# Kernel tuning notes

Measured on AMD Instinct MI355X. Metric: run time of the kernel, lower is better.

## Reference

```python
import jax, jax.numpy as jnp
import numpy as np

N_USERS = 50000
N_ITEMS = 150000
N = N_USERS + N_ITEMS
N_EDGES = 1250000
D = 64
N_LAYERS = 3


def setup_inputs() -> dict:
    key = jax.random.key(0)
    ks = jax.random.split(key, 7)
    edge_src = jax.random.randint(ks[0], (N_EDGES,), 0, N, dtype=jnp.int32)
    edge_dst = jax.random.randint(ks[1], (N_EDGES,), 0, N, dtype=jnp.int32)
    edge_weight = jax.random.uniform(ks[2], (N_EDGES,), dtype=jnp.float32)
    user_emb = jax.random.normal(ks[3], (N_USERS, D), dtype=jnp.float32) * 0.1
    item_emb = jax.random.normal(ks[4], (N_ITEMS, D), dtype=jnp.float32) * 0.1
    # Ws[layer, which_linear] with which_linear in {0: W1 (on L@e), 1: W2 (on (L@e)*e), 2: W3 (on e)}
    Ws = jax.random.normal(ks[5], (N_LAYERS, 3, D, D), dtype=jnp.float32) * (1.0 / np.sqrt(D))
    bs = jnp.zeros((N_LAYERS, 3, D), dtype=jnp.float32)
    return {"edge_src": edge_src, "edge_dst": edge_dst, "edge_weight": edge_weight,
            "user_emb": user_emb, "item_emb": item_emb, "Ws": Ws, "bs": bs}


def _l2_normalize(x):
    # torch.nn.functional.normalize(p=2, dim=1, eps=1e-12)
    n = jnp.sqrt(jnp.sum(x * x, axis=1, keepdims=True))
    return x / jnp.maximum(n, 1e-12)


def reference(edge_src, edge_dst, edge_weight, user_emb, item_emb, Ws, bs):
    e = jnp.concatenate([user_emb, item_emb], axis=0)  # [N, D]
    all_embs = [e]
    for i in range(N_LAYERS):
        # SpMM: term1 = L @ e (COO scatter-add)
        term1 = jax.ops.segment_sum(edge_weight[:, None] * e[edge_src], edge_dst,
                                    num_segments=N)  # [N, D]
        term2 = term1 * e
        inter = (term1 @ Ws[i, 0] + bs[i, 0]
                 + term2 @ Ws[i, 1] + bs[i, 1]
                 + e @ Ws[i, 2] + bs[i, 2])
        inter = jax.nn.leaky_relu(inter, negative_slope=0.01)
        e = _l2_normalize(inter)  # dropout is identity in eval mode
        all_embs.append(e)
    all_embs = jnp.concatenate(all_embs, axis=1)  # [N, 4*D]
    return all_embs[:N_USERS], all_embs[N_USERS:]
```

## Files before the change

kernel.cpp:

```cpp
#include <hip/hip_runtime.h>
#include <hip/hip_bf16.h>

#define NU 50000
#define NI 150000
#define NN 200000
#define NE 1250000
#define DD 64
#define NLAYERS 3
#define SCAN_B 1024
#define NB ((NN + SCAN_B - 1) / SCAN_B)
#define BT_STRIDE 232

typedef __attribute__((ext_vector_type(8))) short bf16x8;
typedef __attribute__((ext_vector_type(4))) float f32x4;

static __device__ __forceinline__ unsigned short f2b(float x) {
  __hip_bfloat16 h = __float2bfloat16(x);
  return *reinterpret_cast<unsigned short*>(&h);
}

static __device__ __forceinline__ unsigned int pack2(float lo, float hi) {
  return (unsigned int)f2b(lo) | ((unsigned int)f2b(hi) << 16);
}

static __device__ __forceinline__ float blo(unsigned int u) { return __uint_as_float(u << 16); }
static __device__ __forceinline__ float bhi(unsigned int u) { return __uint_as_float(u & 0xffff0000u); }

static __device__ __forceinline__ bf16x8 mulbf8(bf16x8 a, bf16x8 b) {
  union { bf16x8 v; unsigned int u[4]; } A, B, R;
  A.v = a; B.v = b;
#pragma unroll
  for (int i = 0; i < 4; ++i) {
    R.u[i] = pack2(blo(A.u[i]) * blo(B.u[i]), bhi(A.u[i]) * bhi(B.u[i]));
  }
  return R.v;
}

__global__ __launch_bounds__(256) void k_zero(int* __restrict__ p) {
  int i = blockIdx.x * 256 + threadIdx.x;
  if (i < NN) p[i] = 0;
}

__global__ __launch_bounds__(256) void k_init(const float4* __restrict__ ue,
                                              const float4* __restrict__ ie,
                                              float4* __restrict__ out4,
                                              uint2* __restrict__ ebf2) {
  int gid = blockIdx.x * 256 + threadIdx.x;
  if (gid >= NN * 16) return;
  int row = gid >> 4, q = gid & 15;
  float4 v = (row < NU) ? ue[(size_t)row * 16 + q] : ie[(size_t)(row - NU) * 16 + q];
  out4[(size_t)row * 64 + q] = v;
  uint2 b; b.x = pack2(v.x, v.y); b.y = pack2(v.z, v.w);
  ebf2[(size_t)row * 16 + q] = b;
}

__global__ __launch_bounds__(256) void k_hist(const int* __restrict__ dst, int* __restrict__ cnt) {
  int e = blockIdx.x * 256 + threadIdx.x;
  if (e < NE) atomicAdd(&cnt[dst[e]], 1);
}

__global__ __launch_bounds__(SCAN_B) void k_scan1(const int* __restrict__ cnt,
                                                  int* __restrict__ local,
                                                  int* __restrict__ btot) {
  __shared__ int sm[SCAN_B];
  int t = threadIdx.x;
  int i = blockIdx.x * SCAN_B + t;
  int v = (i < NN) ? cnt[i] : 0;
  sm[t] = v;
  __syncthreads();
  for (int off = 1; off < SCAN_B; off <<= 1) {
    int x = (t >= off) ? sm[t - off] : 0;
    __syncthreads();
    sm[t] += x;
    __syncthreads();
  }
  if (i < NN) local[i] = sm[t] - v;
  if (t == SCAN_B - 1) btot[blockIdx.x] = sm[t];
}

__global__ __launch_bounds__(256) void k_scan2(int* __restrict__ btot) {
  __shared__ int sm[256];
  int t = threadIdx.x;
  int v = (t < NB) ? btot[t] : 0;
  sm[t] = v;
  __syncthreads();
  for (int off = 1; off < 256; off <<= 1) {
    int x = (t >= off) ? sm[t - off] : 0;
    __syncthreads();
    sm[t] += x;
    __syncthreads();
  }
  if (t < NB) btot[t] = sm[t] - v;
}

__global__ __launch_bounds__(256) void k_finalize(const int* __restrict__ local,
                                                  const int* __restrict__ btot,
                                                  int* __restrict__ row_start,
                                                  int* __restrict__ cursor) {
  int i = blockIdx.x * 256 + threadIdx.x;
  if (i < NN) {
    int v = local[i] + btot[i / SCAN_B];
    row_start[i] = v;
    cursor[i] = v;
  }
  if (i == 0) row_start[NN] = NE;
}

__global__ __launch_bounds__(256) void k_fill(const int* __restrict__ src,
                                              const int* __restrict__ dst,
                                              const float* __restrict__ w,
                                              int* __restrict__ cursor,
                                              int2* __restrict__ csr_pack) {
  int e = blockIdx.x * 256 + threadIdx.x;
  if (e < NE) {
    int p = atomicAdd(&cursor[dst[e]], 1);
    int2 pk; pk.x = src[e]; pk.y = __float_as_int(w[e]);
    csr_pack[p] = pk;
  }
}

__global__ __launch_bounds__(256) void k_spmm(const int* __restrict__ row_start,
                                              const int2* __restrict__ csr_pack,
                                              const unsigned int* __restrict__ ebf,
                                              unsigned int* __restrict__ t1bf) {
  int gid = blockIdx.x * 256 + threadIdx.x;
  int row = gid >> 6;
  if (row >= NN) return;
  int l = gid & 63;
  int h = l >> 5;
  int c = l & 31;
  int s0 = row_start[row];
  int s1 = row_start[row + 1];
  float a0 = 0.f, a1 = 0.f;
  for (int base = s0; base < s1; base += 8) {
    int j0 = base + 0 + h, j1 = base + 2 + h, j2 = base + 4 + h, j3 = base + 6 + h;
    int2 p0 = csr_pack[j0 < s1 ? j0 : 0];
    int2 p1 = csr_pack[j1 < s1 ? j1 : 0];
    int2 p2 = csr_pack[j2 < s1 ? j2 : 0];
    int2 p3 = csr_pack[j3 < s1 ? j3 : 0];
    unsigned int v0 = ebf[(size_t)p0.x * 32 + c];
    unsigned int v1 = ebf[(size_t)p1.x * 32 + c];
    unsigned int v2 = ebf[(size_t)p2.x * 32 + c];
    unsigned int v3 = ebf[(size_t)p3.x * 32 + c];
    float w0 = (j0 < s1) ? __int_as_float(p0.y) : 0.f;
    float w1 = (j1 < s1) ? __int_as_float(p1.y) : 0.f;
    float w2 = (j2 < s1) ? __int_as_float(p2.y) : 0.f;
    float w3 = (j3 < s1) ? __int_as_float(p3.y) : 0.f;
    a0 = fmaf(w0, blo(v0), a0); a1 = fmaf(w0, bhi(v0), a1);
    a0 = fmaf(w1, blo(v1), a0); a1 = fmaf(w1, bhi(v1), a1);
    a0 = fmaf(w2, blo(v2), a0); a1 = fmaf(w2, bhi(v2), a1);
    a0 = fmaf(w3, blo(v3), a0); a1 = fmaf(w3, bhi(v3), a1);
  }
  a0 += __shfl_xor(a0, 32, 64);
  a1 += __shfl_xor(a1, 32, 64);
  if (h == 0) t1bf[(size_t)row * 32 + c] = pack2(a0, a1);
}

__global__ __launch_bounds__(256) void k_row_mfma(const unsigned int* __restrict__ t1bf,
                                                  const unsigned int* __restrict__ ebf,
                                                  const float* __restrict__ Ws,
                                                  const float* __restrict__ bs,
                                                  float* __restrict__ out,
                                                  unsigned short* __restrict__ ebf_next,
                                                  int layer, int wbf) {
  __shared__ unsigned short Bt[64][BT_STRIDE];
  const int tid = threadIdx.x;
  const float* __restrict__ Wl = Ws + (size_t)layer * 3 * 4096;
  {
    int n = tid & 63;
    int jb = (tid >> 6) * 48;
#pragma unroll 4
    for (int j = jb; j < jb + 48; ++j) Bt[n][j] = f2b(Wl[(size_t)j * 64 + n]);
  }
  __syncthreads();

  const int l = tid & 63;
  const int wv = tid >> 6;
  const int g = l >> 4;
  const int li = l & 15;
  const int rowbase = blockIdx.x * 64 + wv * 16;
  const int r = rowbase + li;

  const unsigned short* __restrict__ t1b = reinterpret_cast<const unsigned short*>(t1bf);
  const unsigned short* __restrict__ eb = reinterpret_cast<const unsigned short*>(ebf);
  bf16x8 A0 = *reinterpret_cast<const bf16x8*>(t1b + (size_t)r * 64 + 8 * g);
  bf16x8 A1 = *reinterpret_cast<const bf16x8*>(t1b + (size_t)r * 64 + 32 + 8 * g);
  bf16x8 E0 = *reinterpret_cast<const bf16x8*>(eb + (size_t)r * 64 + 8 * g);
  bf16x8 E1 = *reinterpret_cast<const bf16x8*>(eb + (size_t)r * 64 + 32 + 8 * g);
  bf16x8 T0 = mulbf8(A0, E0);
  bf16x8 T1 = mulbf8(A1, E1);

  const float* __restrict__ bsl = bs + (size_t)layer * 3 * 64;
  f32x4 acc[4];
#pragma unroll
  for (int f = 0; f < 4; ++f) {
    int n = f * 16 + li;
    float bv = bsl[n] + bsl[64 + n] + bsl[128 + n];
    acc[f] = (f32x4){bv, bv, bv, bv};
  }

  bf16x8 Afr[6] = {A0, A1, T0, T1, E0, E1};
#pragma unroll
  for (int s = 0; s < 6; ++s) {
#pragma unroll
    for (int f = 0; f < 4; ++f) {
      const bf16x8 Bf = *reinterpret_cast<const bf16x8*>(&Bt[f * 16 + li][s * 32 + 8 * g]);
      acc[f] = __builtin_amdgcn_mfma_f32_16x16x32_bf16(Afr[s], Bf, acc[f], 0, 0, 0);
    }
  }

  float p[4];
#pragma unroll
  for (int reg = 0; reg < 4; ++reg) {
    float ssum = 0.f;
#pragma unroll
    for (int f = 0; f < 4; ++f) {
      float x = acc[f][reg];
      x = (x >= 0.f) ? x : 0.01f * x;
      acc[f][reg] = x;
      ssum = fmaf(x, x, ssum);
    }
    p[reg] = ssum;
  }
#pragma unroll
  for (int off = 1; off < 16; off <<= 1) {
#pragma unroll
    for (int reg = 0; reg < 4; ++reg) p[reg] += __shfl_xor(p[reg], off, 64);
  }
  float inv[4];
#pragma unroll
  for (int reg = 0; reg < 4; ++reg) inv[reg] = 1.0f / fmaxf(sqrtf(p[reg]), 1e-12f);

  float* __restrict__ ob = out + (size_t)(layer + 1) * 64;
#pragma unroll
  for (int reg = 0; reg < 4; ++reg) {
#pragma unroll
    for (int f = 0; f < 4; ++f) {
      float val = acc[f][reg] * inv[reg];
      ob[(size_t)(rowbase + 4 * g + reg) * 256 + f * 16 + li] = val;
      if (wbf) ebf_next[(size_t)(rowbase + 4 * g + reg) * 64 + f * 16 + li] = f2b(val);
    }
  }
}

extern "C" void kernel_launch(void* const* d_in, const int* in_sizes, int n_in,
                              void* d_out, int out_size, void* d_ws, size_t ws_size,
                              hipStream_t stream) {
  const int* edge_src = (const int*)d_in[0];
  const int* edge_dst = (const int*)d_in[1];
  const float* edge_w = (const float*)d_in[2];
  const float* user_emb = (const float*)d_in[3];
  const float* item_emb = (const float*)d_in[4];
  const float* Ws = (const float*)d_in[5];
  const float* bs = (const float*)d_in[6];
  float* out = (float*)d_out;

  char* w = (char*)d_ws;
  unsigned int* ebfA = (unsigned int*)w; w += (size_t)NN * 32 * 4;
  unsigned int* ebfB = (unsigned int*)w; w += (size_t)NN * 32 * 4;
  unsigned int* t1bf = (unsigned int*)w; w += (size_t)NN * 32 * 4;
  int2* csr_pack = (int2*)w;      w += (size_t)NE * 8;
  int* cnt = (int*)w;             w += (size_t)NN * 4;
  int* local = (int*)w;           w += (size_t)NN * 4;
  int* row_start = (int*)w;       w += (size_t)(NN + 4) * 4;
  int* cursor = (int*)w;          w += (size_t)NN * 4;
  int* btot = (int*)w;            w += 256 * 4;

  k_zero<<<(NN + 255) / 256, 256, 0, stream>>>(cnt);
  k_init<<<(NN * 16 + 255) / 256, 256, 0, stream>>>(
      (const float4*)user_emb, (const float4*)item_emb, (float4*)out, (uint2*)ebfA);
  k_hist<<<(NE + 255) / 256, 256, 0, stream>>>(edge_dst, cnt);
  k_scan1<<<NB, SCAN_B, 0, stream>>>(cnt, local, btot);
  k_scan2<<<1, 256, 0, stream>>>(btot);
  k_finalize<<<(NN + 255) / 256, 256, 0, stream>>>(local, btot, row_start, cursor);
  k_fill<<<(NE + 255) / 256, 256, 0, stream>>>(edge_src, edge_dst, edge_w, cursor, csr_pack);

  k_spmm<<<(NN * 64 + 255) / 256, 256, 0, stream>>>(row_start, csr_pack, ebfA, t1bf);
  k_row_mfma<<<NN / 64, 256, 0, stream>>>(t1bf, ebfA, Ws, bs, out, (unsigned short*)ebfB, 0, 1);
  k_spmm<<<(NN * 64 + 255) / 256, 256, 0, stream>>>(row_start, csr_pack, ebfB, t1bf);
  k_row_mfma<<<NN / 64, 256, 0, stream>>>(t1bf, ebfB, Ws, bs, out, (unsigned short*)ebfA, 1, 1);
  k_spmm<<<(NN * 64 + 255) / 256, 256, 0, stream>>>(row_start, csr_pack, ebfA, t1bf);
  k_row_mfma<<<NN / 64, 256, 0, stream>>>(t1bf, ebfA, Ws, bs, out, (unsigned short*)ebfB, 2, 0);
}
```

Baseline: 415.6 us.

## Vectorize SpMM gathers to 16-byte loads and pretranspose weights to bf16 once

The SpMM kernel now has each wavefront process 8 edges at a time, with 8 lanes per edge each loading a 16-byte chunk of the source row, in place of 4-byte per-lane loads over 2 edges. Partial sums are combined with xor-shuffles and stored as one 16-byte write. A new prep kernel converts and transposes all layer weights to bf16 once, so each MFMA block copies its weight tile into shared memory with vector loads instead of a strided per-element conversion. This cuts gather instruction count and per-block weight-load overhead, at the cost of more shuffle reductions and 8 accumulators per lane.

```diff
diff --git a/kernel.cpp b/kernel.cpp
--- a/kernel.cpp
+++ b/kernel.cpp
@@ -39,6 +39,16 @@
 __global__ __launch_bounds__(256) void k_zero(int* __restrict__ p) {
   int i = blockIdx.x * 256 + threadIdx.x;
   if (i < NN) p[i] = 0;
+}
+
+__global__ __launch_bounds__(256) void k_wprep(const float* __restrict__ Ws,
+                                               unsigned short* __restrict__ WtBf) {
+  int t = blockIdx.x * 256 + threadIdx.x;
+  if (t >= 3 * 64 * 192) return;
+  int j = t % 192;
+  int n = (t / 192) & 63;
+  int lyr = t / (192 * 64);
+  WtBf[t] = f2b(Ws[((size_t)lyr * 3 + (j >> 6)) * 4096 + (size_t)(j & 63) * 64 + n]);
 }
 
 __global__ __launch_bounds__(256) void k_init(const float4* __restrict__ ue,
@@ -126,51 +136,74 @@
   int gid = blockIdx.x * 256 + threadIdx.x;
   int row = gid >> 6;
   if (row >= NN) return;
-  int l = gid & 63;
-  int h = l >> 5;
-  int c = l & 31;
+  const int l = gid & 63;
+  const int eidx = l >> 3;
+  const int cb = l & 7;
   int s0 = row_start[row];
   int s1 = row_start[row + 1];
-  float a0 = 0.f, a1 = 0.f;
-  for (int base = s0; base < s1; base += 8) {
-    int j0 = base + 0 + h, j1 = base + 2 + h, j2 = base + 4 + h, j3 = base + 6 + h;
+
+  float a0 = 0.f, a1 = 0.f, a2 = 0.f, a3 = 0.f, a4 = 0.f, a5 = 0.f, a6 = 0.f, a7 = 0.f;
+
+  if (s0 < s1) {
+    int j0 = s0 + eidx, j1 = s0 + 8 + eidx;
     int2 p0 = csr_pack[j0 < s1 ? j0 : 0];
     int2 p1 = csr_pack[j1 < s1 ? j1 : 0];
-    int2 p2 = csr_pack[j2 < s1 ? j2 : 0];
-    int2 p3 = csr_pack[j3 < s1 ? j3 : 0];
-    unsigned int v0 = ebf[(size_t)p0.x * 32 + c];
-    unsigned int v1 = ebf[(size_t)p1.x * 32 + c];
-    unsigned int v2 = ebf[(size_t)p2.x * 32 + c];
-    unsigned int v3 = ebf[(size_t)p3.x * 32 + c];
+    uint4 v0 = *reinterpret_cast<const uint4*>(ebf + (size_t)p0.x * 32 + cb * 4);
+    uint4 v1 = *reinterpret_cast<const uint4*>(ebf + (size_t)p1.x * 32 + cb * 4);
     float w0 = (j0 < s1) ? __int_as_float(p0.y) : 0.f;
     float w1 = (j1 < s1) ? __int_as_float(p1.y) : 0.f;
-    float w2 = (j2 < s1) ? __int_as_float(p2.y) : 0.f;
-    float w3 = (j3 < s1) ? __int_as_float(p3.y) : 0.f;
-    a0 = fmaf(w0, blo(v0), a0); a1 = fmaf(w0, bhi(v0), a1);
-    a0 = fmaf(w1, blo(v1), a0); a1 = fmaf(w1, bhi(v1), a1);
-    a0 = fmaf(w2, blo(v2), a0); a1 = fmaf(w2, bhi(v2), a1);
-    a0 = fmaf(w3, blo(v3), a0); a1 = fmaf(w3, bhi(v3), a1);
-  }
-  a0 += __shfl_xor(a0, 32, 64);
-  a1 += __shfl_xor(a1, 32, 64);
-  if (h == 0) t1bf[(size_t)row * 32 + c] = pack2(a0, a1);
+    a0 = fmaf(w0, blo(v0.x), a0); a1 = fmaf(w0, bhi(v0.x), a1);
+    a2 = fmaf(w0, blo(v0.y), a2); a3 = fmaf(w0, bhi(v0.y), a3);
+    a4 = fmaf(w0, blo(v0.z), a4); a5 = fmaf(w0, bhi(v0.z), a5);
+    a6 = fmaf(w0, blo(v0.w), a6); a7 = fmaf(w0, bhi(v0.w), a7);
+    a0 = fmaf(w1, blo(v1.x), a0); a1 = fmaf(w1, bhi(v1.x), a1);
+    a2 = fmaf(w1, blo(v1.y), a2); a3 = fmaf(w1, bhi(v1.y), a3);
+    a4 = fmaf(w1, blo(v1.z), a4); a5 = fmaf(w1, bhi(v1.z), a5);
+    a6 = fmaf(w1, blo(v1.w), a6); a7 = fmaf(w1, bhi(v1.w), a7);
+    for (int base = s0 + 16; base < s1; base += 8) {
+      int j = base + eidx;
+      int2 p = csr_pack[j < s1 ? j : 0];
+      uint4 v = *reinterpret_cast<const uint4*>(ebf + (size_t)p.x * 32 + cb * 4);
+      float wt = (j < s1) ? __int_as_float(p.y) : 0.f;
+      a0 = fmaf(wt, blo(v.x), a0); a1 = fmaf(wt, bhi(v.x), a1);
+      a2 = fmaf(wt, blo(v.y), a2); a3 = fmaf(wt, bhi(v.y), a3);
+      a4 = fmaf(wt, blo(v.z), a4); a5 = fmaf(wt, bhi(v.z), a5);
+      a6 = fmaf(wt, blo(v.w), a6); a7 = fmaf(wt, bhi(v.w), a7);
+    }
+  }
+
+  a0 += __shfl_xor(a0, 8, 64);  a0 += __shfl_xor(a0, 16, 64);  a0 += __shfl_xor(a0, 32, 64);
+  a1 += __shfl_xor(a1, 8, 64);  a1 += __shfl_xor(a1, 16, 64);  a1 += __shfl_xor(a1, 32, 64);
+  a2 += __shfl_xor(a2, 8, 64);  a2 += __shfl_xor(a2, 16, 64);  a2 += __shfl_xor(a2, 32, 64);
+  a3 += __shfl_xor(a3, 8, 64);  a3 += __shfl_xor(a3, 16, 64);  a3 += __shfl_xor(a3, 32, 64);
+  a4 += __shfl_xor(a4, 8, 64);  a4 += __shfl_xor(a4, 16, 64);  a4 += __shfl_xor(a4, 32, 64);
+  a5 += __shfl_xor(a5, 8, 64);  a5 += __shfl_xor(a5, 16, 64);  a5 += __shfl_xor(a5, 32, 64);
+  a6 += __shfl_xor(a6, 8, 64);  a6 += __shfl_xor(a6, 16, 64);  a6 += __shfl_xor(a6, 32, 64);
+  a7 += __shfl_xor(a7, 8, 64);  a7 += __shfl_xor(a7, 16, 64);  a7 += __shfl_xor(a7, 32, 64);
+
+  if (l < 8) {
+    uint4 st;
+    st.x = pack2(a0, a1); st.y = pack2(a2, a3); st.z = pack2(a4, a5); st.w = pack2(a6, a7);
+    *reinterpret_cast<uint4*>(t1bf + (size_t)row * 32 + l * 4) = st;
+  }
 }
 
 __global__ __launch_bounds__(256) void k_row_mfma(const unsigned int* __restrict__ t1bf,
                                                   const unsigned int* __restrict__ ebf,
-                                                  const float* __restrict__ Ws,
+                                                  const unsigned short* __restrict__ WtBf,
                                                   const float* __restrict__ bs,
                                                   float* __restrict__ out,
                                                   unsigned short* __restrict__ ebf_next,
                                                   int layer, int wbf) {
   __shared__ unsigned short Bt[64][BT_STRIDE];
   const int tid = threadIdx.x;
-  const float* __restrict__ Wl = Ws + (size_t)layer * 3 * 4096;
   {
-    int n = tid & 63;
-    int jb = (tid >> 6) * 48;
-#pragma unroll 4
-    for (int j = jb; j < jb + 48; ++j) Bt[n][j] = f2b(Wl[(size_t)j * 64 + n]);
+    const uint4* __restrict__ src = reinterpret_cast<const uint4*>(WtBf + (size_t)layer * 64 * 192);
+#pragma unroll
+    for (int ch = tid; ch < 1536; ch += 256) {
+      int rown = ch / 24, k = ch % 24;
+      *reinterpret_cast<uint4*>(&Bt[rown][k * 8]) = src[ch];
+    }
   }
   __syncthreads();
 
@@ -260,6 +293,7 @@
   unsigned int* ebfB = (unsigned int*)w; w += (size_t)NN * 32 * 4;
   unsigned int* t1bf = (unsigned int*)w; w += (size_t)NN * 32 * 4;
   int2* csr_pack = (int2*)w;      w += (size_t)NE * 8;
+  unsigned short* WtBf = (unsigned short*)w; w += (size_t)3 * 64 * 192 * 2;
   int* cnt = (int*)w;             w += (size_t)NN * 4;
   int* local = (int*)w;           w += (size_t)NN * 4;
   int* row_start = (int*)w;       w += (size_t)(NN + 4) * 4;
@@ -267,6 +301,7 @@
   int* btot = (int*)w;            w += 256 * 4;
 
   k_zero<<<(NN + 255) / 256, 256, 0, stream>>>(cnt);
+  k_wprep<<<(3 * 64 * 192 + 255) / 256, 256, 0, stream>>>(Ws, WtBf);
   k_init<<<(NN * 16 + 255) / 256, 256, 0, stream>>>(
       (const float4*)user_emb, (const float4*)item_emb, (float4*)out, (uint2*)ebfA);
   k_hist<<<(NE + 255) / 256, 256, 0, stream>>>(edge_dst, cnt);
@@ -276,9 +311,9 @@
   k_fill<<<(NE + 255) / 256, 256, 0, stream>>>(edge_src, edge_dst, edge_w, cursor, csr_pack);
 
   k_spmm<<<(NN * 64 + 255) / 256, 256, 0, stream>>>(row_start, csr_pack, ebfA, t1bf);
-  k_row_mfma<<<NN / 64, 256, 0, stream>>>(t1bf, ebfA, Ws, bs, out, (unsigned short*)ebfB, 0, 1);
+  k_row_mfma<<<NN / 64, 256, 0, stream>>>(t1bf, ebfA, WtBf, bs, out, (unsigned short*)ebfB, 0, 1);
   k_spmm<<<(NN * 64 + 255) / 256, 256, 0, stream>>>(row_start, csr_pack, ebfB, t1bf);
-  k_row_mfma<<<NN / 64, 256, 0, stream>>>(t1bf, ebfB, Ws, bs, out, (unsigned short*)ebfA, 1, 1);
+  k_row_mfma<<<NN / 64, 256, 0, stream>>>(t1bf, ebfB, WtBf, bs, out, (unsigned short*)ebfA, 1, 1);
   k_spmm<<<(NN * 64 + 255) / 256, 256, 0, stream>>>(row_start, csr_pack, ebfA, t1bf);
-  k_row_mfma<<<NN / 64, 256, 0, stream>>>(t1bf, ebfA, Ws, bs, out, (unsigned short*)ebfB, 2, 0);
-}
+  k_row_mfma<<<NN / 64, 256, 0, stream>>>(t1bf, ebfA, WtBf, bs, out, (unsigned short*)ebfB, 2, 0);
+}
```

After: 411.0 us. Within noise of the previous version (-1.1%).
